# Optimization experiments

Measured on AMD Instinct MI355X. Metric: run time of the kernel, lower is better.

Reference implementation:

```python
import jax, jax.numpy as jnp
import numpy as np

D_MODEL = 1024
NUM_HEADS = 16
DEPTH = D_MODEL // NUM_HEADS


def setup_inputs() -> dict:
    key = jax.random.key(0)
    ks = jax.random.split(key, 10)
    B, LQ, LK = 4, 2048, 2048
    # xavier_uniform bound for square [d,d] weight
    bound = float(np.sqrt(6.0 / (D_MODEL + D_MODEL)))
    def w(k):
        return jax.random.uniform(k, (D_MODEL, D_MODEL), jnp.float32, -bound, bound)
    return {
        "query": jax.random.normal(ks[0], (B, LQ, D_MODEL), jnp.float32),
        "value": jax.random.normal(ks[1], (B, LK, D_MODEL), jnp.float32),
        "wq": w(ks[2]), "bq": jnp.zeros((D_MODEL,), jnp.float32),
        "wk": w(ks[3]), "bk": jnp.zeros((D_MODEL,), jnp.float32),
        "wv": w(ks[4]), "bv": jnp.zeros((D_MODEL,), jnp.float32),
        "wo": w(ks[5]), "bo": jnp.zeros((D_MODEL,), jnp.float32),
    }


def _split_heads(x, B):
    # [B, L, d_model] -> [B, H, L, depth]
    return x.reshape(B, -1, NUM_HEADS, DEPTH).transpose(0, 2, 1, 3)


def reference(query, value, wq, bq, wk, bk, wv, bv, wo, bo):
    B = query.shape[0]
    # torch nn.Linear: y = x @ W.T + b
    q = _split_heads(query @ wq.T + bq, B)          # [B,H,Lq,depth]
    k = _split_heads(value @ wk.T + bk, B)          # [B,H,Lk,depth]
    v = _split_heads(value @ wv.T + bv, B)          # [B,H,Lk,depth]
    scale = jnp.sqrt(jnp.asarray(DEPTH, dtype=q.dtype))
    scores = jnp.einsum("bhqd,bhkd->bhqk", q, k) / scale
    attn = jax.nn.softmax(scores, axis=-1)
    ctx = jnp.einsum("bhqk,bhkd->bhqd", attn, v)    # [B,H,Lq,depth]
    ctx = ctx.transpose(0, 2, 1, 3).reshape(B, -1, D_MODEL)
    return ctx @ wo.T + bo
```

## Files before the change

### kernel.cpp

```cpp
#include <hip/hip_runtime.h>
#include <hip/hip_bf16.h>

typedef unsigned short u16;
typedef unsigned int u32;
typedef __attribute__((ext_vector_type(8))) short bf16x8;
typedef __attribute__((ext_vector_type(4))) float f32x4;

#define MFMA16(a, b, c) __builtin_amdgcn_mfma_f32_16x16x32_bf16(a, b, c, 0, 0, 0)

#define QSCALE 0.18033688011112042f

__device__ inline u16 f2b(float f) {
    union { float f; unsigned int i; } v;
    v.f = f;
    unsigned int r = v.i + 0x7fffu + ((v.i >> 16) & 1u);
    return (u16)(r >> 16);
}
__device__ inline u32 fbits(float f) {
    union { float f; u32 i; } v; v.f = f; return v.i;
}
__device__ inline u32 pack2_trunc(float f0, float f1) {
    return __builtin_amdgcn_perm(fbits(f1), fbits(f0), 0x07060302u);
}

__device__ inline void glds16(const u16* g, u16* l) {
    __builtin_amdgcn_global_load_lds(
        (const __attribute__((address_space(1))) unsigned int*)g,
        (__attribute__((address_space(3))) unsigned int*)l, 16, 0, 0);
}

__global__ __launch_bounds__(256) void cvt_all(
    const float* __restrict__ q, const float* __restrict__ v,
    const float* __restrict__ wq, const float* __restrict__ wk,
    const float* __restrict__ wv, const float* __restrict__ wo,
    u16* __restrict__ qb, u16* __restrict__ vb,
    u16* __restrict__ wqb, u16* __restrict__ wkb,
    u16* __restrict__ wvb, u16* __restrict__ wob)
{
    int flat = blockIdx.x;
    const float* x; u16* y; int off;
    if (flat < 8192) {
        x = flat < 4096 ? q : v;
        y = flat < 4096 ? qb : vb;
        off = flat & 4095;
    } else {
        int s = (flat - 8192) >> 9;
        off = (flat - 8192) & 511;
        x = s == 0 ? wq : (s == 1 ? wk : (s == 2 ? wv : wo));
        y = s == 0 ? wqb : (s == 1 ? wkb : (s == 2 ? wvb : wob));
    }
    int i = (off * 256 + threadIdx.x) * 8;
    float4 a = *(const float4*)(x + i);
    float4 b = *(const float4*)(x + i + 4);
    u16 o[8] = { f2b(a.x), f2b(a.y), f2b(a.z), f2b(a.w),
                 f2b(b.x), f2b(b.y), f2b(b.z), f2b(b.w) };
    *(uint4*)(y + i) = *(uint4*)o;
}

__global__ __launch_bounds__(256) void gemm_proj(
    const u16* __restrict__ qb, const u16* __restrict__ vb,
    const u16* __restrict__ wqb, const u16* __restrict__ wkb,
    const u16* __restrict__ wvb,
    const float* __restrict__ bq, const float* __restrict__ bk,
    const float* __restrict__ bv,
    u16* __restrict__ Qp, u16* __restrict__ Kp, u16* __restrict__ Vp,
    int M, int K)
{
    const int sel = blockIdx.y >> 3;
    const int n0 = (blockIdx.y & 7) * 128;
    const u16* A = sel ? vb : qb;
    const u16* W = sel == 0 ? wqb : (sel == 1 ? wkb : wvb);
    const float* bias = sel == 0 ? bq : (sel == 1 ? bk : bv);
    u16* C = sel == 0 ? Qp : (sel == 1 ? Kp : Vp);
    const float cscale = sel == 0 ? QSCALE : 1.0f;

    __shared__ __align__(16) u16 As[128 * 32];
    __shared__ __align__(16) u16 Bs[128 * 32];

    const int tid  = threadIdx.x;
    const int wave = tid >> 6, lane = tid & 63;
    const int quad = lane >> 4, l16 = lane & 15;
    const int m0 = blockIdx.x * 128;
    const int wm = (wave >> 1) * 64, wn = (wave & 1) * 64;
    const int r0 = lane >> 2;
    const int c0 = (lane & 3) * 8;

    f32x4 acc[4][4] = {};

    for (int k0 = 0; k0 < K; k0 += 32) {
        __syncthreads();
        {
            int ra = wave * 16 + r0;
            glds16(&A[(size_t)(m0 + ra) * K + k0 + c0],      &As[ra * 32 + c0]);
            glds16(&A[(size_t)(m0 + 64 + ra) * K + k0 + c0], &As[(64 + ra) * 32 + c0]);
            glds16(&W[(size_t)(n0 + ra) * K + k0 + c0],      &Bs[ra * 32 + c0]);
            glds16(&W[(size_t)(n0 + 64 + ra) * K + k0 + c0], &Bs[(64 + ra) * 32 + c0]);
        }
        __syncthreads();

        bf16x8 af[4], bfr[4];
#pragma unroll
        for (int mi = 0; mi < 4; ++mi)
            af[mi] = *(const bf16x8*)(&As[(wm + mi * 16 + l16) * 32 + quad * 8]);
#pragma unroll
        for (int ni = 0; ni < 4; ++ni)
            bfr[ni] = *(const bf16x8*)(&Bs[(wn + ni * 16 + l16) * 32 + quad * 8]);
#pragma unroll
        for (int mi = 0; mi < 4; ++mi)
#pragma unroll
            for (int ni = 0; ni < 4; ++ni)
                acc[mi][ni] = MFMA16(af[mi], bfr[ni], acc[mi][ni]);
    }

#pragma unroll
    for (int mi = 0; mi < 4; ++mi) {
#pragma unroll
        for (int ni = 0; ni < 4; ++ni) {
            int col = n0 + wn + ni * 16 + l16;
            float bv2 = bias[col];
#pragma unroll
            for (int r = 0; r < 4; ++r) {
                int row = m0 + wm + mi * 16 + quad * 4 + r;
                C[(size_t)row * 1024 + col] = f2b((acc[mi][ni][r] + bv2) * cscale);
            }
        }
    }
}

__global__ __launch_bounds__(256) void gemm_out(
    const u16* __restrict__ A, const u16* __restrict__ B,
    const float* __restrict__ bias, float* __restrict__ C,
    int M, int N, int K)
{
    __shared__ __align__(16) u16 As[128 * 32];
    __shared__ __align__(16) u16 Bs[128 * 32];

    const int tid  = threadIdx.x;
    const int wave = tid >> 6, lane = tid & 63;
    const int quad = lane >> 4, l16 = lane & 15;
    const int m0 = blockIdx.x * 128, n0 = blockIdx.y * 128;
    const int wm = (wave >> 1) * 64, wn = (wave & 1) * 64;
    const int r0 = lane >> 2;
    const int c0 = (lane & 3) * 8;

    f32x4 acc[4][4] = {};

    for (int k0 = 0; k0 < K; k0 += 32) {
        __syncthreads();
        {
            int ra = wave * 16 + r0;
            glds16(&A[(size_t)(m0 + ra) * K + k0 + c0],      &As[ra * 32 + c0]);
            glds16(&A[(size_t)(m0 + 64 + ra) * K + k0 + c0], &As[(64 + ra) * 32 + c0]);
            glds16(&B[(size_t)(n0 + ra) * K + k0 + c0],      &Bs[ra * 32 + c0]);
            glds16(&B[(size_t)(n0 + 64 + ra) * K + k0 + c0], &Bs[(64 + ra) * 32 + c0]);
        }
        __syncthreads();

        bf16x8 af[4], bfr[4];
#pragma unroll
        for (int mi = 0; mi < 4; ++mi)
            af[mi] = *(const bf16x8*)(&As[(wm + mi * 16 + l16) * 32 + quad * 8]);
#pragma unroll
        for (int ni = 0; ni < 4; ++ni)
            bfr[ni] = *(const bf16x8*)(&Bs[(wn + ni * 16 + l16) * 32 + quad * 8]);
#pragma unroll
        for (int mi = 0; mi < 4; ++mi)
#pragma unroll
            for (int ni = 0; ni < 4; ++ni)
                acc[mi][ni] = MFMA16(af[mi], bfr[ni], acc[mi][ni]);
    }

#pragma unroll
    for (int mi = 0; mi < 4; ++mi) {
#pragma unroll
        for (int ni = 0; ni < 4; ++ni) {
            int col = n0 + wn + ni * 16 + l16;
            float bv = bias[col];
#pragma unroll
            for (int r = 0; r < 4; ++r) {
                int row = m0 + wm + mi * 16 + quad * 4 + r;
                C[(size_t)row * N + col] = acc[mi][ni][r] + bv;
            }
        }
    }
}

__global__ __launch_bounds__(256) void transpose_v(
    const u16* __restrict__ Vp, u16* __restrict__ VT)
{
    __shared__ u16 T[64 * 66];
    const int tid = threadIdx.x;
    const int l0 = blockIdx.x * 64, d0 = blockIdx.y * 64, b = blockIdx.z;

#pragma unroll
    for (int i = 0; i < 2; ++i) {
        int ch = tid + i * 256;
        int lrow = ch >> 3, c8 = (ch & 7) * 8;
        uint4 vv = *(const uint4*)(&Vp[((size_t)b * 2048 + l0 + lrow) * 1024 + d0 + c8]);
        const u16* vp = (const u16*)&vv;
#pragma unroll
        for (int j = 0; j < 8; ++j) T[lrow * 66 + c8 + j] = vp[j];
    }
    __syncthreads();
#pragma unroll
    for (int i = 0; i < 2; ++i) {
        int ch = tid + i * 256;
        int drow = ch >> 3, l8 = (ch & 7) * 8;
        u16 o[8];
#pragma unroll
        for (int j = 0; j < 8; ++j) o[j] = T[(l8 + j) * 66 + drow];
        *(uint4*)(&VT[((size_t)b * 1024 + d0 + drow) * 2048 + l0 + l8]) = *(uint4*)o;
    }
}

__global__ __launch_bounds__(256, 4) void attn(
    const u16* __restrict__ Q, const u16* __restrict__ K,
    const u16* __restrict__ VT, u16* __restrict__ O,
    int LQ, int LK)
{
    const int tid  = threadIdx.x;
    const int wave = tid >> 6, lane = tid & 63;
    const int quad = lane >> 4, l16 = lane & 15;
    const int flat = blockIdx.x;
    const int xcd = flat & 7, slot = flat >> 3;
    const int bh = xcd * 8 + (slot >> 4);
    const int q0 = (slot & 15) * 128;
    const int b = bh >> 4, h = bh & 15;
    const size_t qbase = ((size_t)b * LQ + q0) * 1024 + h * 64;
    const size_t kbase = ((size_t)b * LK) * 1024 + h * 64;
    const size_t vtbase = ((size_t)b * 1024 + h * 64) * 2048;

    __shared__ __align__(16) u16 Ks[64 * 72];
    __shared__ __align__(16) u16 VTs[64 * 72];
    __shared__ __align__(16) u16 Ps[4][32 * 40];

    bf16x8 qf[2][2];
#pragma unroll
    for (int mi = 0; mi < 2; ++mi)
#pragma unroll
        for (int ks = 0; ks < 2; ++ks)
            qf[mi][ks] = *(const bf16x8*)(
                &Q[qbase + (size_t)(wave * 32 + mi * 16 + l16) * 1024 + ks * 32 + quad * 8]);

    const bf16x8 vones = { 0x3F80, 0x3F80, 0x3F80, 0x3F80,
                           0x3F80, 0x3F80, 0x3F80, 0x3F80 };

    f32x4 oacc[2][5] = {};

    const int row0 = tid >> 3, c8 = (tid & 7) * 8;
    const int row1 = row0 + 32;
    const u16* kp0 = K + kbase + (size_t)row0 * 1024 + c8;
    const u16* kp1 = K + kbase + (size_t)row1 * 1024 + c8;
    const u16* vp0 = VT + vtbase + (size_t)row0 * 2048 + c8;
    const u16* vp1 = VT + vtbase + (size_t)row1 * 2048 + c8;

    uint4 kreg0 = *(const uint4*)kp0;
    uint4 kreg1 = *(const uint4*)kp1;
    uint4 vreg0 = *(const uint4*)vp0;
    uint4 vreg1 = *(const uint4*)vp1;

    for (int kt = 0; kt < LK; kt += 64) {
        __syncthreads();
        *(uint4*)(&Ks[row0 * 72 + c8])  = kreg0;
        *(uint4*)(&Ks[row1 * 72 + c8])  = kreg1;
        *(uint4*)(&VTs[row0 * 72 + c8]) = vreg0;
        *(uint4*)(&VTs[row1 * 72 + c8]) = vreg1;
        __syncthreads();

        if (kt + 64 < LK) {
            kp0 += 64 * 1024; kp1 += 64 * 1024; vp0 += 64; vp1 += 64;
            kreg0 = *(const uint4*)kp0;
            kreg1 = *(const uint4*)kp1;
            vreg0 = *(const uint4*)vp0;
            vreg1 = *(const uint4*)vp1;
        }

        f32x4 st[4][2] = {};
#pragma unroll
        for (int ks = 0; ks < 2; ++ks) {
            bf16x8 kf[4];
#pragma unroll
            for (int ni = 0; ni < 4; ++ni)
                kf[ni] = *(const bf16x8*)(&Ks[(ni * 16 + l16) * 72 + ks * 32 + quad * 8]);
            __builtin_amdgcn_s_setprio(1);
#pragma unroll
            for (int ni = 0; ni < 4; ++ni)
#pragma unroll
                for (int mi = 0; mi < 2; ++mi)
                    st[ni][mi] = MFMA16(kf[ni], qf[mi][ks], st[ni][mi]);
            __builtin_amdgcn_s_setprio(0);
        }

#pragma unroll
        for (int ks = 0; ks < 2; ++ks) {
#pragma unroll
            for (int mi = 0; mi < 2; ++mi)
#pragma unroll
                for (int ni2 = 0; ni2 < 2; ++ni2) {
                    const f32x4 s4 = st[ks * 2 + ni2][mi];
                    float p0 = __builtin_amdgcn_exp2f(s4[0]);
                    float p1 = __builtin_amdgcn_exp2f(s4[1]);
                    float p2 = __builtin_amdgcn_exp2f(s4[2]);
                    float p3 = __builtin_amdgcn_exp2f(s4[3]);
                    uint2 w;
                    w.x = pack2_trunc(p0, p1);
                    w.y = pack2_trunc(p2, p3);
                    *(uint2*)(&Ps[wave][(mi * 16 + l16) * 40 + ni2 * 16 + quad * 4]) = w;
                }

            bf16x8 vf[4];
#pragma unroll
            for (int nd = 0; nd < 4; ++nd)
                vf[nd] = *(const bf16x8*)(&VTs[(nd * 16 + l16) * 72 + ks * 32 + quad * 8]);
            __builtin_amdgcn_s_setprio(1);
#pragma unroll
            for (int mi = 0; mi < 2; ++mi) {
                bf16x8 pf = *(const bf16x8*)(&Ps[wave][(mi * 16 + l16) * 40 + quad * 8]);
#pragma unroll
                for (int nd = 0; nd < 4; ++nd)
                    oacc[mi][nd] = MFMA16(pf, vf[nd], oacc[mi][nd]);
                oacc[mi][4] = MFMA16(pf, vones, oacc[mi][4]);
            }
            __builtin_amdgcn_s_setprio(0);
        }
    }

#pragma unroll
    for (int mi = 0; mi < 2; ++mi)
#pragma unroll
        for (int r = 0; r < 4; ++r) {
            float inv = 1.0f / oacc[mi][4][r];
            int row = q0 + wave * 32 + mi * 16 + quad * 4 + r;
            size_t rb = ((size_t)b * LQ + row) * 1024 + h * 64;
#pragma unroll
            for (int nd = 0; nd < 4; ++nd)
                O[rb + nd * 16 + l16] = f2b(oacc[mi][nd][r] * inv);
        }
}

extern "C" void kernel_launch(void* const* d_in, const int* in_sizes, int n_in,
                              void* d_out, int out_size, void* d_ws, size_t ws_size,
                              hipStream_t stream) {
    const float* query = (const float*)d_in[0];
    const float* value = (const float*)d_in[1];
    const float* wq = (const float*)d_in[2];
    const float* bq = (const float*)d_in[3];
    const float* wk = (const float*)d_in[4];
    const float* bk = (const float*)d_in[5];
    const float* wv = (const float*)d_in[6];
    const float* bv = (const float*)d_in[7];
    const float* wo = (const float*)d_in[8];
    const float* bo = (const float*)d_in[9];

    const int B = 4, LQ = 2048, LK = 2048, D = 1024;
    const int M = B * LQ;
    const int mat = M * D;
    const int wsz = D * D;

    u16* ws  = (u16*)d_ws;
    u16* qb  = ws;
    u16* vb  = qb + mat;
    u16* wqb = vb + mat;
    u16* wkb = wqb + wsz;
    u16* wvb = wkb + wsz;
    u16* wob = wvb + wsz;
    u16* Qp  = wob + wsz;
    u16* Kp  = Qp + mat;
    u16* Vp  = Kp + mat;
    u16* VT  = Vp + mat;
    u16* Cp  = Vp;

    dim3 blk(256);

    cvt_all<<<dim3(10240), blk, 0, stream>>>(
        query, value, wq, wk, wv, wo, qb, vb, wqb, wkb, wvb, wob);

    gemm_proj<<<dim3(M / 128, 24), blk, 0, stream>>>(
        qb, vb, wqb, wkb, wvb, bq, bk, bv, Qp, Kp, Vp, M, D);

    transpose_v<<<dim3(32, 16, 4), blk, 0, stream>>>(Vp, VT);

    attn<<<dim3(1024), blk, 0, stream>>>(Qp, Kp, VT, Cp, LQ, LK);

    gemm_out<<<dim3(M / 128, D / 128), blk, 0, stream>>>(Cp, wob, bo, (float*)d_out, M, D, D);
}
```

Before: 353.3 us.

## Remap GEMM blocks per XCD for L2 locality and drop attention register prefetch

Both GEMM kernels switch to a 1D grid, and the block index is remapped so that the eight blocks landing on each XCD share the same group of M tiles. The intent is better per-XCD L2 reuse of the A rows. The attention kernel no longer prefetches the next K/V tile into registers; it loads global memory straight into LDS each iteration. That lowers register pressure, but global load latency is no longer overlapped with compute.

```diff
diff --git a/kernel.cpp b/kernel.cpp
--- a/kernel.cpp
+++ b/kernel.cpp
@@ -66,8 +66,12 @@
     u16* __restrict__ Qp, u16* __restrict__ Kp, u16* __restrict__ Vp,
     int M, int K)
 {
-    const int sel = blockIdx.y >> 3;
-    const int n0 = (blockIdx.y & 7) * 128;
+    const int flat = blockIdx.x;
+    const int xcd = flat & 7, idx = flat >> 3;
+    const int mt  = xcd * 8 + (idx & 7);
+    const int yy  = idx >> 3;
+    const int sel = yy >> 3;
+    const int n0 = (yy & 7) * 128;
     const u16* A = sel ? vb : qb;
     const u16* W = sel == 0 ? wqb : (sel == 1 ? wkb : wvb);
     const float* bias = sel == 0 ? bq : (sel == 1 ? bk : bv);
@@ -80,7 +84,7 @@
     const int tid  = threadIdx.x;
     const int wave = tid >> 6, lane = tid & 63;
     const int quad = lane >> 4, l16 = lane & 15;
-    const int m0 = blockIdx.x * 128;
+    const int m0 = mt * 128;
     const int wm = (wave >> 1) * 64, wn = (wave & 1) * 64;
     const int r0 = lane >> 2;
     const int c0 = (lane & 3) * 8;
@@ -135,10 +139,14 @@
     __shared__ __align__(16) u16 As[128 * 32];
     __shared__ __align__(16) u16 Bs[128 * 32];
 
+    const int flat = blockIdx.x;
+    const int xcd = flat & 7, idx = flat >> 3;
+    const int mt  = xcd * 8 + (idx & 7);
+    const int m0 = mt * 128, n0 = (idx >> 3) * 128;
+
     const int tid  = threadIdx.x;
     const int wave = tid >> 6, lane = tid & 63;
     const int quad = lane >> 4, l16 = lane & 15;
-    const int m0 = blockIdx.x * 128, n0 = blockIdx.y * 128;
     const int wm = (wave >> 1) * 64, wn = (wave & 1) * 64;
     const int r0 = lane >> 2;
     const int c0 = (lane & 3) * 8;
@@ -247,33 +255,18 @@
 
     f32x4 oacc[2][5] = {};
 
-    const int row0 = tid >> 3, c8 = (tid & 7) * 8;
-    const int row1 = row0 + 32;
-    const u16* kp0 = K + kbase + (size_t)row0 * 1024 + c8;
-    const u16* kp1 = K + kbase + (size_t)row1 * 1024 + c8;
-    const u16* vp0 = VT + vtbase + (size_t)row0 * 2048 + c8;
-    const u16* vp1 = VT + vtbase + (size_t)row1 * 2048 + c8;
-
-    uint4 kreg0 = *(const uint4*)kp0;
-    uint4 kreg1 = *(const uint4*)kp1;
-    uint4 vreg0 = *(const uint4*)vp0;
-    uint4 vreg1 = *(const uint4*)vp1;
-
     for (int kt = 0; kt < LK; kt += 64) {
         __syncthreads();
-        *(uint4*)(&Ks[row0 * 72 + c8])  = kreg0;
-        *(uint4*)(&Ks[row1 * 72 + c8])  = kreg1;
-        *(uint4*)(&VTs[row0 * 72 + c8]) = vreg0;
-        *(uint4*)(&VTs[row1 * 72 + c8]) = vreg1;
-        __syncthreads();
-
-        if (kt + 64 < LK) {
-            kp0 += 64 * 1024; kp1 += 64 * 1024; vp0 += 64; vp1 += 64;
-            kreg0 = *(const uint4*)kp0;
-            kreg1 = *(const uint4*)kp1;
-            vreg0 = *(const uint4*)vp0;
-            vreg1 = *(const uint4*)vp1;
-        }
+#pragma unroll
+        for (int i = 0; i < 2; ++i) {
+            int ch = tid + i * 256;
+            int row = ch >> 3, c8 = (ch & 7) * 8;
+            *(uint4*)(&Ks[row * 72 + c8]) =
+                *(const uint4*)(&K[kbase + (size_t)(kt + row) * 1024 + c8]);
+            *(uint4*)(&VTs[row * 72 + c8]) =
+                *(const uint4*)(&VT[vtbase + (size_t)row * 2048 + kt + c8]);
+        }
+        __syncthreads();
 
         f32x4 st[4][2] = {};
 #pragma unroll
@@ -375,12 +368,12 @@
     cvt_all<<<dim3(10240), blk, 0, stream>>>(
         query, value, wq, wk, wv, wo, qb, vb, wqb, wkb, wvb, wob);
 
-    gemm_proj<<<dim3(M / 128, 24), blk, 0, stream>>>(
+    gemm_proj<<<dim3(1536), blk, 0, stream>>>(
         qb, vb, wqb, wkb, wvb, bq, bk, bv, Qp, Kp, Vp, M, D);
 
     transpose_v<<<dim3(32, 16, 4), blk, 0, stream>>>(Vp, VT);
 
     attn<<<dim3(1024), blk, 0, stream>>>(Qp, Kp, VT, Cp, LQ, LK);
 
-    gemm_out<<<dim3(M / 128, D / 128), blk, 0, stream>>>(Cp, wob, bo, (float*)d_out, M, D, D);
-}
+    gemm_out<<<dim3(512), blk, 0, stream>>>(Cp, wob, bo, (float*)d_out, M, D, D);
+}
```

Result: faster. 328.5 us (-7.0%).
